# Kernel tuning notes

Measured on AMD Instinct MI355X. Metric: run time of the kernel, lower is better.

## Reference

```python
import jax, jax.numpy as jnp
import numpy as np

B, T, C = 4, 2048, 1024
H, D = 16, 64          # n_head, head_size; H*D == C
FF = 4 * C             # compute_layer_scaling * n_embed
EPS = 1e-5


def layernorm(x, g, b):
    mu = jnp.mean(x, axis=-1, keepdims=True)
    var = jnp.var(x, axis=-1, keepdims=True)
    return (x - mu) * jax.lax.rsqrt(var + EPS) * g + b


def setup_inputs() -> dict:
    key = jax.random.key(0)
    ks = jax.random.split(key, 12)
    s_c = 1.0 / np.sqrt(C)
    s_ff = 1.0 / np.sqrt(FF)
    return {
        "x": jax.random.normal(ks[0], (B, T, C), dtype=jnp.float32),
        # per-head Q/K/V weights, stacked: [H, C, D] (Linear with bias=False)
        "Wq": jax.random.normal(ks[1], (H, C, D), dtype=jnp.float32) * s_c,
        "Wk": jax.random.normal(ks[2], (H, C, D), dtype=jnp.float32) * s_c,
        "Wv": jax.random.normal(ks[3], (H, C, D), dtype=jnp.float32) * s_c,
        "Wproj": jax.random.normal(ks[4], (C, C), dtype=jnp.float32) * s_c,
        "bproj": jnp.zeros((C,), dtype=jnp.float32),
        "W1": jax.random.normal(ks[5], (C, FF), dtype=jnp.float32) * s_c,
        "b1": jnp.zeros((FF,), dtype=jnp.float32),
        "W2": jax.random.normal(ks[6], (FF, FF), dtype=jnp.float32) * s_ff,
        "b2": jnp.zeros((FF,), dtype=jnp.float32),
        "W3": jax.random.normal(ks[7], (FF, C), dtype=jnp.float32) * s_ff,
        "b3": jnp.zeros((C,), dtype=jnp.float32),
        "ln1_g": jnp.ones((C,), dtype=jnp.float32),
        "ln1_b": jnp.zeros((C,), dtype=jnp.float32),
        "ln2_g": jnp.ones((C,), dtype=jnp.float32),
        "ln2_b": jnp.zeros((C,), dtype=jnp.float32),
    }


def reference(x, Wq, Wk, Wv, Wproj, bproj, W1, b1, W2, b2, W3, b3,
              ln1_g, ln1_b, ln2_g, ln2_b):
    # --- multi-head causal self-attention (pre-LN) ---
    h = layernorm(x, ln1_g, ln1_b)
    q = jnp.einsum("btc,hcd->bhtd", h, Wq)
    k = jnp.einsum("btc,hcd->bhtd", h, Wk)
    v = jnp.einsum("btc,hcd->bhtd", h, Wv)
    # NOTE: original scales by n_embed**-0.5 (C from x.shape), not head_size
    scores = jnp.einsum("bhtd,bhsd->bhts", q, k) * (C ** -0.5)
    causal = jnp.tril(jnp.ones((T, T), dtype=bool))
    scores = jnp.where(causal, scores, -jnp.inf)
    wei = jax.nn.softmax(scores, axis=-1)          # dropout p=0 -> identity
    attn = jnp.einsum("bhts,bhsd->bhtd", wei, v)
    attn = attn.transpose(0, 2, 1, 3).reshape(B, T, C)  # concat heads
    x = x + attn @ Wproj + bproj
    # --- feed-forward (pre-LN): C -> FF -> relu -> FF -> relu -> C ---
    h2 = layernorm(x, ln2_g, ln2_b)
    h2 = jax.nn.relu(h2 @ W1 + b1)
    h2 = jax.nn.relu(h2 @ W2 + b2)
    x = x + h2 @ W3 + b3
    return x
```

## Files before the change

### kernel.cpp

```cpp
#include <hip/hip_runtime.h>

typedef __bf16 bf16;
typedef bf16  bf16x8 __attribute__((ext_vector_type(8)));
typedef bf16  bf16x4 __attribute__((ext_vector_type(4)));
typedef float f32x4  __attribute__((ext_vector_type(4)));

#define T_SEQ 2048

__device__ __forceinline__ void gload_lds16(const bf16* g, bf16* l) {
    __builtin_amdgcn_global_load_lds(
        (const __attribute__((address_space(1))) unsigned int*)g,
        (__attribute__((address_space(3))) unsigned int*)l,
        16, 0, 0);
}

#define VMCNT(n) asm volatile("s_waitcnt vmcnt(" #n ")" ::: "memory")
#define BAR() do { asm volatile("" ::: "memory"); __builtin_amdgcn_s_barrier(); \
                   asm volatile("" ::: "memory"); } while (0)

__global__ __launch_bounds__(256) void transpose_f32_bf16(
    const float* __restrict__ in, bf16* __restrict__ out, int R, int Cc, int ldo)
{
    __shared__ float tile[32][33];
    const int bx = blockIdx.x * 32;
    const int by = blockIdx.y * 32;
    const long bi = (long)blockIdx.z * R * Cc;
    const long bo = (long)blockIdx.z * Cc * ldo;
    const int tx = threadIdx.x, ty = threadIdx.y;
#pragma unroll
    for (int i = 0; i < 4; ++i)
        tile[ty + i * 8][tx] = in[bi + (long)(by + ty + i * 8) * Cc + bx + tx];
    __syncthreads();
#pragma unroll
    for (int i = 0; i < 4; ++i)
        out[bo + (long)(bx + ty + i * 8) * ldo + by + tx] = (bf16)tile[tx][ty + i * 8];
}

__global__ __launch_bounds__(256) void transpose_bf16(
    const bf16* __restrict__ in, bf16* __restrict__ out, int ldi, int ldo)
{
    __shared__ bf16 tile[32][33];
    const int bx = blockIdx.x * 32;
    const int by = blockIdx.y * 32;
    const int tx = threadIdx.x, ty = threadIdx.y;
#pragma unroll
    for (int i = 0; i < 4; ++i)
        tile[ty + i * 8][tx] = in[(long)(by + ty + i * 8) * ldi + bx + tx];
    __syncthreads();
#pragma unroll
    for (int i = 0; i < 4; ++i)
        out[(long)(bx + ty + i * 8) * ldo + by + tx] = tile[tx][ty + i * 8];
}

__global__ __launch_bounds__(256) void ln_kernel(
    const float* __restrict__ x, const float* __restrict__ g,
    const float* __restrict__ bb, bf16* __restrict__ out)
{
    const long row = blockIdx.x;
    const int tid = threadIdx.x;
    const float4 v = ((const float4*)(x + row * 1024))[tid];
    float s  = v.x + v.y + v.z + v.w;
    float s2 = v.x * v.x + v.y * v.y + v.z * v.z + v.w * v.w;
#pragma unroll
    for (int off = 32; off >= 1; off >>= 1) {
        s  += __shfl_xor(s,  off, 64);
        s2 += __shfl_xor(s2, off, 64);
    }
    __shared__ float red[8];
    const int wid = tid >> 6;
    if ((tid & 63) == 0) { red[wid] = s; red[4 + wid] = s2; }
    __syncthreads();
    s  = red[0] + red[1] + red[2] + red[3];
    s2 = red[4] + red[5] + red[6] + red[7];
    const float mu   = s * (1.f / 1024.f);
    const float rstd = rsqrtf(s2 * (1.f / 1024.f) - mu * mu + 1e-5f);
    const float4 gv = ((const float4*)g)[tid];
    const float4 bv = ((const float4*)bb)[tid];
    bf16x4 ov;
    ov[0] = (bf16)((v.x - mu) * rstd * gv.x + bv.x);
    ov[1] = (bf16)((v.y - mu) * rstd * gv.y + bv.y);
    ov[2] = (bf16)((v.z - mu) * rstd * gv.z + bv.z);
    ov[3] = (bf16)((v.w - mu) * rstd * gv.w + bv.w);
    *(bf16x4*)(out + row * 1024 + tid * 4) = ov;
}

__global__ __launch_bounds__(256) void ln_kernel_b(
    const bf16* __restrict__ x, const float* __restrict__ g,
    const float* __restrict__ bb, bf16* __restrict__ out)
{
    const long row = blockIdx.x;
    const int tid = threadIdx.x;
    const bf16x4 vb = ((const bf16x4*)(x + row * 1024))[tid];
    const float v0 = (float)vb[0], v1 = (float)vb[1];
    const float v2 = (float)vb[2], v3 = (float)vb[3];
    float s  = v0 + v1 + v2 + v3;
    float s2 = v0 * v0 + v1 * v1 + v2 * v2 + v3 * v3;
#pragma unroll
    for (int off = 32; off >= 1; off >>= 1) {
        s  += __shfl_xor(s,  off, 64);
        s2 += __shfl_xor(s2, off, 64);
    }
    __shared__ float red[8];
    const int wid = tid >> 6;
    if ((tid & 63) == 0) { red[wid] = s; red[4 + wid] = s2; }
    __syncthreads();
    s  = red[0] + red[1] + red[2] + red[3];
    s2 = red[4] + red[5] + red[6] + red[7];
    const float mu   = s * (1.f / 1024.f);
    const float rstd = rsqrtf(s2 * (1.f / 1024.f) - mu * mu + 1e-5f);
    const float4 gv = ((const float4*)g)[tid];
    const float4 bv = ((const float4*)bb)[tid];
    bf16x4 ov;
    ov[0] = (bf16)((v0 - mu) * rstd * gv.x + bv.x);
    ov[1] = (bf16)((v1 - mu) * rstd * gv.y + bv.y);
    ov[2] = (bf16)((v2 - mu) * rstd * gv.z + bv.z);
    ov[3] = (bf16)((v3 - mu) * rstd * gv.w + bv.w);
    *(bf16x4*)(out + row * 1024 + tid * 4) = ov;
}

#define LOADA(BUFP, QM) do {                                                   \
    const char* ab_ = (BUFP) + (size_t)((wr * 64 + (QM) * 128 + fr) * 128);    \
    _Pragma("unroll") for (int m_ = 0; m_ < 4; ++m_) {                         \
        af[m_][0] = *(const bf16x8*)(ab_ + m_ * 2048 + so0);                   \
        af[m_][1] = *(const bf16x8*)(ab_ + m_ * 2048 + so1); } } while (0)

#define LOADB(BUFP, QN, DST) do {                                              \
    const char* bb_ = (BUFP) + (size_t)((wc * 32 + (QN) * 128 + fr) * 128);    \
    _Pragma("unroll") for (int n_ = 0; n_ < 2; ++n_) {                         \
        DST[n_][0] = *(const bf16x8*)(bb_ + n_ * 2048 + so0);                  \
        DST[n_][1] = *(const bf16x8*)(bb_ + n_ * 2048 + so1); } } while (0)

#define MMA(ACC, BSET) do { __builtin_amdgcn_s_setprio(1);                     \
    _Pragma("unroll") for (int m_ = 0; m_ < 4; ++m_)                           \
    _Pragma("unroll") for (int n_ = 0; n_ < 2; ++n_) {                         \
        ACC[m_][n_] = __builtin_amdgcn_mfma_f32_16x16x32_bf16(                 \
            af[m_][0], BSET[n_][0], ACC[m_][n_], 0, 0, 0);                     \
        ACC[m_][n_] = __builtin_amdgcn_mfma_f32_16x16x32_bf16(                 \
            af[m_][1], BSET[n_][1], ACC[m_][n_], 0, 0, 0); }                   \
    __builtin_amdgcn_s_setprio(0); } while (0)

#define TB_DEEP(W1N, W3N, ISSN, ISSC) do {                                     \
    const char* abuf = cAs + ((size_t)cur << 15);                              \
    const char* bbuf = cBs + ((size_t)cur << 15);                              \
    const long kb  = (long)(k + 1) * 64;                                       \
    const long kb2 = (long)(k + 2) * 64;                                       \
    LOADA(abuf, 0);                                                            \
    LOADB(bbuf, 0, bfv0);                                                      \
    if (ISSN) stageB(nxt, 0, kb);                                 \
    BAR(); MMA(a00, bfv0); BAR();                                              \
    LOADB(bbuf, 1, bfv1);                                                      \
    if (ISSN) stageA(nxt, 1, kb);                                 \
    VMCNT(W1N);                                                                \
    BAR(); MMA(a01, bfv1); BAR();                                              \
    LOADA(abuf, 1);                                                            \
    if (ISSC) stageA(cur, 0, kb2);                                \
    BAR(); MMA(a11, bfv1); BAR();                                              \
    if (ISSC) stageB(cur, 1, kb2);                                \
    VMCNT(W3N);                                                                \
    BAR(); MMA(a10, bfv0); BAR(); } while (0)

template <int MODE>
__global__ __launch_bounds__(512, 1) void gemm256(
    const bf16* __restrict__ A, const bf16* __restrict__ Bt,
    const float* __restrict__ bias, const float* __restrict__ resid,
    void* __restrict__ outp, int M, int N, int K, int nbn)
{
    extern __shared__ __align__(16) char smem[];
    char* cAs = smem;
    char* cBs = smem + 65536;

    const int tid = threadIdx.x;
    const int wid = tid >> 6, lane = tid & 63;
    const int wr = wid >> 2, wc = wid & 3;
    const int fr = lane & 15, fq = lane >> 4;

    const int nwg = gridDim.x;
    const int cpx = nwg >> 3;
    const int b0  = blockIdx.x;
    const int bid = (b0 & 7) * cpx + (b0 >> 3);
    const long bm = bid / nbn, bn = bid % nbn;
    const long bmrow = bm * 256, bnrow = bn * 256;

    const int srow0 = wid * 8 + (lane >> 3);
    const int sslot = (lane & 7) ^ (lane >> 3);
    auto stageA = [&](int buf, int h, long kt) {
        const bf16* g = A + (size_t)(bmrow + h * 128 + srow0) * K + kt + sslot * 8;
        char* l = cAs + ((size_t)buf << 15) + h * 16384 + (size_t)wid * 1024;
        gload_lds16(g, (bf16*)l);
        gload_lds16(g + (size_t)64 * K, (bf16*)(l + 8192));
    };
    auto stageB = [&](int buf, int h, long kt) {
        const bf16* g = Bt + (size_t)(bnrow + h * 128 + srow0) * K + kt + sslot * 8;
        char* l = cBs + ((size_t)buf << 15) + h * 16384 + (size_t)wid * 1024;
        gload_lds16(g, (bf16*)l);
        gload_lds16(g + (size_t)64 * K, (bf16*)(l + 8192));
    };

    const int sx  = fr & 7;
    const int so0 = ((fq) ^ sx) * 16;
    const int so1 = ((4 + fq) ^ sx) * 16;

    bf16x8 af[4][2], bfv0[2][2], bfv1[2][2];
    f32x4 a00[4][2], a01[4][2], a11[4][2], a10[4][2];
#pragma unroll
    for (int m = 0; m < 4; ++m)
#pragma unroll
        for (int n = 0; n < 2; ++n) {
            a00[m][n] = {0.f, 0.f, 0.f, 0.f}; a01[m][n] = {0.f, 0.f, 0.f, 0.f};
            a11[m][n] = {0.f, 0.f, 0.f, 0.f}; a10[m][n] = {0.f, 0.f, 0.f, 0.f};
        }

    stageA(0, 0, 0);
    stageB(0, 1, 0);
    stageB(0, 0, 0);
    stageA(0, 1, 0);
    stageA(1, 0, 64);
    stageB(1, 1, 64);
    VMCNT(6);
    BAR();

    const int NT = K >> 6;
    int cur, nxt;
    int k = 0;
    for (; k < NT - 2; ++k) {
        cur = k & 1; nxt = cur ^ 1;
        TB_DEEP(8, 6, true, true);
    }
    cur = k & 1; nxt = cur ^ 1;
    TB_DEEP(8, 2, true, false);
    ++k;
    cur = k & 1; nxt = cur ^ 1;
    TB_DEEP(0, 0, false, false);

    auto writeQ = [&](f32x4 (&acc)[4][2], int QM, int QN) {
#pragma unroll
        for (int m = 0; m < 4; ++m) {
            const long row0 = bmrow + wr * 64 + QM * 128 + m * 16 + fq * 4;
#pragma unroll
            for (int n = 0; n < 2; ++n) {
                const long col = bnrow + wc * 32 + QN * 128 + n * 16 + fr;
                const float bv = (MODE == 0) ? 0.f : bias[col];
#pragma unroll
                for (int j = 0; j < 4; ++j) {
                    const long row = row0 + j;
                    float v = acc[m][n][j] + bv;
                    if (MODE == 1) v = fmaxf(v, 0.f);
                    if (MODE == 2) {
                        v += resid[row * N + col];
                        ((float*)outp)[row * N + col] = v;
                    } else {
                        ((bf16*)outp)[row * N + col] = (bf16)v;
                    }
                }
            }
        }
    };
    writeQ(a00, 0, 0); writeQ(a01, 0, 1); writeQ(a11, 1, 1); writeQ(a10, 1, 0);
}

#define TILE_BODY_N(PRE, LAST) do {                                            \
    const char* abuf = cAs + ((size_t)cur << 15);                              \
    const char* bbuf = cBs + ((size_t)cur << 14);                              \
    const long kn = (long)(k + 1) * 64;                                        \
    LOADA(abuf, 0);                                                            \
    LOADB(bbuf, 0, bfv);                                                       \
    if (PRE) { stageA(nxt, 0, kn); stageB(nxt, kn); stageA(nxt, 1, kn);        \
               VMCNT(6); }                                                     \
    else     { VMCNT(0); }                                                     \
    BAR(); MMA(aq0, bfv); BAR();                                               \
    LOADA(abuf, 1);                                                            \
    if (PRE) { VMCNT(2); }                                                     \
    if (!LAST) { BAR(); }                                                      \
    MMA(aq1, bfv);                                                             \
    if (!LAST) { BAR(); } } while (0)

template <int MODE>
__global__ __launch_bounds__(512, 2) void gemm256n(
    const bf16* __restrict__ A, const bf16* __restrict__ Bt,
    const float* __restrict__ bias, const void* __restrict__ resid,
    void* __restrict__ outp, int M, int N, int K, int nbn)
{
    extern __shared__ __align__(16) char smem[];
    char* cAs = smem;
    char* cBs = smem + 65536;

    const int tid = threadIdx.x;
    const int wid = tid >> 6, lane = tid & 63;
    const int wr = wid >> 2, wc = wid & 3;
    const int fr = lane & 15, fq = lane >> 4;

    const int nwg = gridDim.x;
    const int cpx = nwg >> 3;
    const int b0  = blockIdx.x;
    const int bid = (b0 & 7) * cpx + (b0 >> 3);
    const long bm = bid / nbn, bn = bid % nbn;
    const long bmrow = bm * 256, bnrow = bn * 128;

    const int srow0 = wid * 8 + (lane >> 3);
    const int sslot = (lane & 7) ^ (lane >> 3);
    auto stageA = [&](int buf, int h, long kt) {
        const bf16* g = A + (size_t)(bmrow + h * 128 + srow0) * K + kt + sslot * 8;
        char* l = cAs + ((size_t)buf << 15) + h * 16384 + (size_t)wid * 1024;
        gload_lds16(g, (bf16*)l);
        gload_lds16(g + (size_t)64 * K, (bf16*)(l + 8192));
    };
    auto stageB = [&](int buf, long kt) {
        const bf16* g = Bt + (size_t)(bnrow + srow0) * K + kt + sslot * 8;
        char* l = cBs + ((size_t)buf << 14) + (size_t)wid * 1024;
        gload_lds16(g, (bf16*)l);
        gload_lds16(g + (size_t)64 * K, (bf16*)(l + 8192));
    };

    const int sx  = fr & 7;
    const int so0 = ((fq) ^ sx) * 16;
    const int so1 = ((4 + fq) ^ sx) * 16;

    bf16x8 af[4][2], bfv[2][2];
    f32x4 aq0[4][2], aq1[4][2];
#pragma unroll
    for (int m = 0; m < 4; ++m)
#pragma unroll
        for (int n = 0; n < 2; ++n) {
            aq0[m][n] = {0.f, 0.f, 0.f, 0.f};
            aq1[m][n] = {0.f, 0.f, 0.f, 0.f};
        }

    stageA(0, 0, 0); stageB(0, 0); stageA(0, 1, 0);
    VMCNT(2);
    BAR();

    const int NT = K >> 6;
    int cur = 0, nxt = 1;
    int k = 0;
    for (; k < NT - 1; ++k) {
        cur = k & 1; nxt = cur ^ 1;
        TILE_BODY_N(true, false);
    }
    cur = k & 1; nxt = cur ^ 1;
    TILE_BODY_N(false, true);

    auto writeQ = [&](f32x4 (&acc)[4][2], int QM) {
#pragma unroll
        for (int m = 0; m < 4; ++m) {
            const long row0 = bmrow + wr * 64 + QM * 128 + m * 16 + fq * 4;
#pragma unroll
            for (int n = 0; n < 2; ++n) {
                const long col = bnrow + wc * 32 + n * 16 + fr;
                const float bv = (MODE == 0) ? 0.f : bias[col];
#pragma unroll
                for (int j = 0; j < 4; ++j) {
                    const long row = row0 + j;
                    float v = acc[m][n][j] + bv;
                    if (MODE == 3) {
                        v += ((const float*)resid)[row * N + col];
                        ((bf16*)outp)[row * N + col] = (bf16)v;
                    } else if (MODE == 4) {
                        v += (float)((const bf16*)resid)[row * N + col];
                        ((float*)outp)[row * N + col] = v;
                    } else {
                        ((bf16*)outp)[row * N + col] = (bf16)v;
                    }
                }
            }
        }
    };
    writeQ(aq0, 0); writeQ(aq1, 1);
}

__device__ __forceinline__ void sm_part(
    f32x4* s, float* mj, f32x4* o, f32x4& o_l, bf16* Pp,
    int fr, int fq, int qloc, bool diag)
{
    float v[4][4], mxj[4];
#pragma unroll
    for (int j = 0; j < 4; ++j) {
        const int qg = qloc + fq * 4 + j;
        v[0][j] = s[0][j] * 0.03125f;
        v[1][j] = s[1][j] * 0.03125f;
        v[2][j] = s[2][j] * 0.03125f;
        v[3][j] = s[3][j] * 0.03125f;
        if (diag) {
            if (fr      > qg) v[0][j] = -1e30f;
            if (16 + fr > qg) v[1][j] = -1e30f;
            if (32 + fr > qg) v[2][j] = -1e30f;
            if (48 + fr > qg) v[3][j] = -1e30f;
        }
        float mx = fmaxf(fmaxf(v[0][j], v[1][j]), fmaxf(v[2][j], v[3][j]));
#pragma unroll
        for (int off = 1; off <= 8; off <<= 1) mx = fmaxf(mx, __shfl_xor(mx, off, 16));
        mxj[j] = mx;
    }
    float need = fmaxf(fmaxf(mxj[0] - mj[0], mxj[1] - mj[1]),
                       fmaxf(mxj[2] - mj[2], mxj[3] - mj[3]));
    if (__any(need > 8.f)) {
#pragma unroll
        for (int j = 0; j < 4; ++j) {
            const float mn   = fmaxf(mj[j], mxj[j]);
            const float corr = __expf(mj[j] - mn);
            mj[j] = mn;
#pragma unroll
            for (int nd = 0; nd < 4; ++nd) o[nd][j] *= corr;
            o_l[j] *= corr;
        }
    }
#pragma unroll
    for (int j = 0; j < 4; ++j) {
        bf16* prow = Pp + (fq * 4 + j) * 72;
        prow[fr]      = (bf16)__expf(v[0][j] - mj[j]);
        prow[16 + fr] = (bf16)__expf(v[1][j] - mj[j]);
        prow[32 + fr] = (bf16)__expf(v[2][j] - mj[j]);
        prow[48 + fr] = (bf16)__expf(v[3][j] - mj[j]);
    }
}

__device__ __forceinline__ void attn_step(
    const bf16* __restrict__ Ks, const bf16* __restrict__ Vt,
    bf16* __restrict__ Pp, const bf16x8* qf,
    f32x4* o, f32x4& o_l, float* mj, const bf16x8 onesf,
    int fr, int fq, int qloc, bool diag)
{
    f32x4 s[4];
#pragma unroll
    for (int n = 0; n < 4; ++n) s[n] = {0.f, 0.f, 0.f, 0.f};
    __builtin_amdgcn_s_setprio(1);
#pragma unroll
    for (int n = 0; n < 4; ++n) {
        const int t  = n * 16 + fr;
        const int sw = ((t ^ (t >> 3)) & 7) << 4;
        const bf16x8 kf0 = *(const bf16x8*)((const char*)Ks + t * 128 + ((fq * 16) ^ sw));
        const bf16x8 kf1 = *(const bf16x8*)((const char*)Ks + t * 128 + ((64 + fq * 16) ^ sw));
        s[n] = __builtin_amdgcn_mfma_f32_16x16x32_bf16(qf[0], kf0, s[n], 0, 0, 0);
        s[n] = __builtin_amdgcn_mfma_f32_16x16x32_bf16(qf[1], kf1, s[n], 0, 0, 0);
    }
    __builtin_amdgcn_s_setprio(0);
    sm_part(s, mj, o, o_l, Pp, fr, fq, qloc, diag);
    asm volatile("s_waitcnt lgkmcnt(0)" ::: "memory");
    __builtin_amdgcn_sched_barrier(0);
    const bf16x8 pf0 = *(const bf16x8*)(Pp + fr * 72 + fq * 8);
    const bf16x8 pf1 = *(const bf16x8*)(Pp + fr * 72 + 32 + fq * 8);
    __builtin_amdgcn_s_setprio(1);
#pragma unroll
    for (int nd = 0; nd < 4; ++nd) {
        const int dd = nd * 16 + fr;
        const int sw = ((dd ^ (dd >> 3)) & 7) << 4;
        const bf16x8 vf0 = *(const bf16x8*)((const char*)Vt + dd * 128 + ((fq * 16) ^ sw));
        const bf16x8 vf1 = *(const bf16x8*)((const char*)Vt + dd * 128 + ((64 + fq * 16) ^ sw));
        o[nd] = __builtin_amdgcn_mfma_f32_16x16x32_bf16(pf0, vf0, o[nd], 0, 0, 0);
        o[nd] = __builtin_amdgcn_mfma_f32_16x16x32_bf16(pf1, vf1, o[nd], 0, 0, 0);
    }
    o_l = __builtin_amdgcn_mfma_f32_16x16x32_bf16(pf0, onesf, o_l, 0, 0, 0);
    o_l = __builtin_amdgcn_mfma_f32_16x16x32_bf16(pf1, onesf, o_l, 0, 0, 0);
    __builtin_amdgcn_s_setprio(0);
}

__device__ __forceinline__ void attn_step2(
    const bf16* __restrict__ Ks, const bf16* __restrict__ Vt,
    bf16* __restrict__ PpA, bf16* __restrict__ PpB,
    const bf16x8* qfA, const bf16x8* qfB,
    f32x4* oA, f32x4& olA, float* mA,
    f32x4* oB, f32x4& olB, float* mB,
    const bf16x8 onesf, int fr, int fq, int qloc, bool diagA)
{
    f32x4 sA[4], sB[4];
#pragma unroll
    for (int n = 0; n < 4; ++n) { sA[n] = {0.f, 0.f, 0.f, 0.f}; sB[n] = {0.f, 0.f, 0.f, 0.f}; }
    __builtin_amdgcn_s_setprio(1);
#pragma unroll
    for (int n = 0; n < 4; ++n) {
        const int t  = n * 16 + fr;
        const int sw = ((t ^ (t >> 3)) & 7) << 4;
        const bf16x8 kf0 = *(const bf16x8*)((const char*)Ks + t * 128 + ((fq * 16) ^ sw));
        const bf16x8 kf1 = *(const bf16x8*)((const char*)Ks + t * 128 + ((64 + fq * 16) ^ sw));
        sA[n] = __builtin_amdgcn_mfma_f32_16x16x32_bf16(qfA[0], kf0, sA[n], 0, 0, 0);
        sA[n] = __builtin_amdgcn_mfma_f32_16x16x32_bf16(qfA[1], kf1, sA[n], 0, 0, 0);
        sB[n] = __builtin_amdgcn_mfma_f32_16x16x32_bf16(qfB[0], kf0, sB[n], 0, 0, 0);
        sB[n] = __builtin_amdgcn_mfma_f32_16x16x32_bf16(qfB[1], kf1, sB[n], 0, 0, 0);
    }
    __builtin_amdgcn_s_setprio(0);
    sm_part(sA, mA, oA, olA, PpA, fr, fq, qloc, diagA);
    sm_part(sB, mB, oB, olB, PpB, fr, fq, qloc, false);
    asm volatile("s_waitcnt lgkmcnt(0)" ::: "memory");
    __builtin_amdgcn_sched_barrier(0);
    const bf16x8 pfA0 = *(const bf16x8*)(PpA + fr * 72 + fq * 8);
    const bf16x8 pfA1 = *(const bf16x8*)(PpA + fr * 72 + 32 + fq * 8);
    const bf16x8 pfB0 = *(const bf16x8*)(PpB + fr * 72 + fq * 8);
    const bf16x8 pfB1 = *(const bf16x8*)(PpB + fr * 72 + 32 + fq * 8);
    __builtin_amdgcn_s_setprio(1);
#pragma unroll
    for (int nd = 0; nd < 4; ++nd) {
        const int dd = nd * 16 + fr;
        const int sw = ((dd ^ (dd >> 3)) & 7) << 4;
        const bf16x8 vf0 = *(const bf16x8*)((const char*)Vt + dd * 128 + ((fq * 16) ^ sw));
        const bf16x8 vf1 = *(const bf16x8*)((const char*)Vt + dd * 128 + ((64 + fq * 16) ^ sw));
        oA[nd] = __builtin_amdgcn_mfma_f32_16x16x32_bf16(pfA0, vf0, oA[nd], 0, 0, 0);
        oA[nd] = __builtin_amdgcn_mfma_f32_16x16x32_bf16(pfA1, vf1, oA[nd], 0, 0, 0);
        oB[nd] = __builtin_amdgcn_mfma_f32_16x16x32_bf16(pfB0, vf0, oB[nd], 0, 0, 0);
        oB[nd] = __builtin_amdgcn_mfma_f32_16x16x32_bf16(pfB1, vf1, oB[nd], 0, 0, 0);
    }
    olA = __builtin_amdgcn_mfma_f32_16x16x32_bf16(pfA0, onesf, olA, 0, 0, 0);
    olA = __builtin_amdgcn_mfma_f32_16x16x32_bf16(pfA1, onesf, olA, 0, 0, 0);
    olB = __builtin_amdgcn_mfma_f32_16x16x32_bf16(pfB0, onesf, olB, 0, 0, 0);
    olB = __builtin_amdgcn_mfma_f32_16x16x32_bf16(pfB1, onesf, olB, 0, 0, 0);
    __builtin_amdgcn_s_setprio(0);
}

__global__ __launch_bounds__(256) void attn_kernel(
    const bf16* __restrict__ qkv, const bf16* __restrict__ vt,
    bf16* __restrict__ out)
{
    const int pair = blockIdx.x;
    const int h = blockIdx.y, b = blockIdx.z;
    const int tid = threadIdx.x, wid = tid >> 6, lane = tid & 63;
    const int fr = lane & 15, fq = lane >> 4;
    const int jA = pair, jB = 31 - pair;
    const bf16* baseQ = qkv + ((long)b * T_SEQ) * 3072 + h * 64;
    const bf16* baseK = baseQ + 1024;
    const bf16* baseV = vt + (long)(h * 64) * 8192 + (long)b * T_SEQ;

    __shared__ __align__(16) bf16 Ks[2][64 * 64];
    __shared__ __align__(16) bf16 Vs[2][64 * 64];
    __shared__ __align__(16) bf16 Plds[2][4][16 * 72];

    const int qrA = jA * 64 + wid * 16 + fr;
    const int qrB = jB * 64 + wid * 16 + fr;
    bf16x8 qfA[2], qfB[2];
#pragma unroll
    for (int kk = 0; kk < 2; ++kk) {
        qfA[kk] = *(const bf16x8*)(baseQ + (long)qrA * 3072 + kk * 32 + fq * 8);
        qfB[kk] = *(const bf16x8*)(baseQ + (long)qrB * 3072 + kk * 32 + fq * 8);
    }

    bf16x8 onesf;
    {
        const bf16 ov = (fr == 0) ? (bf16)1.f : (bf16)0.f;
#pragma unroll
        for (int e = 0; e < 8; ++e) onesf[e] = ov;
    }

    f32x4 oA[4], oB[4], olA, olB;
    float mA[4], mB[4];
#pragma unroll
    for (int nd = 0; nd < 4; ++nd) { oA[nd] = {0.f, 0.f, 0.f, 0.f}; oB[nd] = {0.f, 0.f, 0.f, 0.f}; }
    olA = {0.f, 0.f, 0.f, 0.f}; olB = {0.f, 0.f, 0.f, 0.f};
#pragma unroll
    for (int j = 0; j < 4; ++j) { mA[j] = -1e30f; mB[j] = -1e30f; }

    const int t_p0 = wid * 16 + (lane >> 3);
    const int t_p1 = t_p0 + 8;
    const int kcb0 = ((lane & 7) * 16) ^ (((t_p0 ^ (t_p0 >> 3)) & 7) << 4);
    const int kcb1 = ((lane & 7) * 16) ^ (((t_p1 ^ (t_p1 >> 3)) & 7) << 4);

    bf16* PA = &Plds[0][wid][0];
    bf16* PB = &Plds[1][wid][0];

    auto stage = [&](int buf, int c) {
        const long s0 = (long)c * 64;
        gload_lds16(baseK + (s0 + t_p0) * 3072 + (kcb0 >> 1), &Ks[buf][(wid * 2) * 512]);
        gload_lds16(baseK + (s0 + t_p1) * 3072 + (kcb1 >> 1), &Ks[buf][(wid * 2 + 1) * 512]);
        gload_lds16(baseV + (long)t_p0 * 8192 + s0 + (kcb0 >> 1), &Vs[buf][(wid * 2) * 512]);
        gload_lds16(baseV + (long)t_p1 * 8192 + s0 + (kcb1 >> 1), &Vs[buf][(wid * 2 + 1) * 512]);
    };

    const int nch = jB + 1;
    stage(0, 0);
    for (int c = 0; c < nch; ++c) {
        const int cur = c & 1;
        if (c + 1 < nch) { stage(cur ^ 1, c + 1); VMCNT(4); }
        else             { VMCNT(0); }
        BAR();
        if (c <= jA)
            attn_step2(Ks[cur], Vs[cur], PA, PB, qfA, qfB,
                       oA, olA, mA, oB, olB, mB, onesf, fr, fq, wid * 16, c == jA);
        else
            attn_step(Ks[cur], Vs[cur], PB, qfB, oB, olB, mB, onesf,
                      fr, fq, wid * 16, c == jB);
        BAR();
    }

#pragma unroll
    for (int j = 0; j < 4; ++j) {
        const float lA = __shfl(olA[j], lane & 48, 64);
        const float lB = __shfl(olB[j], lane & 48, 64);
        const float rA = 1.f / lA, rB = 1.f / lB;
        const long rowA = (long)b * T_SEQ + jA * 64 + wid * 16 + fq * 4 + j;
        const long rowB = (long)b * T_SEQ + jB * 64 + wid * 16 + fq * 4 + j;
#pragma unroll
        for (int nd = 0; nd < 4; ++nd) {
            out[rowA * 1024 + h * 64 + nd * 16 + fr] = (bf16)(oA[nd][j] * rA);
            out[rowB * 1024 + h * 64 + nd * 16 + fr] = (bf16)(oB[nd][j] * rB);
        }
    }
}

extern "C" void kernel_launch(void* const* d_in, const int* in_sizes, int n_in,
                              void* d_out, int out_size, void* d_ws, size_t ws_size,
                              hipStream_t stream)
{
    const float* x     = (const float*)d_in[0];
    const float* Wq    = (const float*)d_in[1];
    const float* Wk    = (const float*)d_in[2];
    const float* Wv    = (const float*)d_in[3];
    const float* Wproj = (const float*)d_in[4];
    const float* bproj = (const float*)d_in[5];
    const float* W1    = (const float*)d_in[6];
    const float* b1    = (const float*)d_in[7];
    const float* W2    = (const float*)d_in[8];
    const float* b2    = (const float*)d_in[9];
    const float* W3    = (const float*)d_in[10];
    const float* b3    = (const float*)d_in[11];
    const float* ln1g  = (const float*)d_in[12];
    const float* ln1b  = (const float*)d_in[13];
    const float* ln2g  = (const float*)d_in[14];
    const float* ln2b  = (const float*)d_in[15];

    char* ws = (char*)d_ws;
    size_t off = 0;
    auto alloc = [&](size_t bytes) {
        void* p = ws + off;
        off += (bytes + 255) & ~(size_t)255;
        return p;
    };
    bf16* Wqkv_t  = (bf16*)alloc(3072ul * 1024 * 2);
    bf16* Wproj_t = (bf16*)alloc(1024ul * 1024 * 2);
    bf16* W1_t    = (bf16*)alloc(4096ul * 1024 * 2);
    bf16* W2_t    = (bf16*)alloc(4096ul * 4096 * 2);
    bf16* W3_t    = (bf16*)alloc(1024ul * 4096 * 2);
    bf16* hbuf    = (bf16*)alloc(8192ul * 1024 * 2);
    bf16* x1b     = (bf16*)alloc(8192ul * 1024 * 2);
    bf16* a1      = (bf16*)alloc(8192ul * 4096 * 2);
    char* R1      = (char*)alloc(8192ul * 4096 * 2);
    bf16* qkvb    = (bf16*)R1;
    bf16* attnb   = (bf16*)(R1 + 8192ul * 3072 * 2);
    bf16* a2      = (bf16*)R1;
    bf16* vt      = a1;

    hipFuncSetAttribute(reinterpret_cast<const void*>(&gemm256<1>),
                        hipFuncAttributeMaxDynamicSharedMemorySize, 131072);
    hipFuncSetAttribute(reinterpret_cast<const void*>(&gemm256n<0>),
                        hipFuncAttributeMaxDynamicSharedMemorySize, 98304);
    hipFuncSetAttribute(reinterpret_cast<const void*>(&gemm256n<3>),
                        hipFuncAttributeMaxDynamicSharedMemorySize, 98304);
    hipFuncSetAttribute(reinterpret_cast<const void*>(&gemm256n<4>),
                        hipFuncAttributeMaxDynamicSharedMemorySize, 98304);

    const dim3 tb(32, 8);
    transpose_f32_bf16<<<dim3(2, 32, 16), tb, 0, stream>>>(Wq, Wqkv_t,                1024, 64, 1024);
    transpose_f32_bf16<<<dim3(2, 32, 16), tb, 0, stream>>>(Wk, Wqkv_t + 1024l * 1024, 1024, 64, 1024);
    transpose_f32_bf16<<<dim3(2, 32, 16), tb, 0, stream>>>(Wv, Wqkv_t + 2048l * 1024, 1024, 64, 1024);
    transpose_f32_bf16<<<dim3(32, 32, 1),   tb, 0, stream>>>(Wproj, Wproj_t, 1024, 1024, 1024);
    transpose_f32_bf16<<<dim3(128, 32, 1),  tb, 0, stream>>>(W1, W1_t, 1024, 4096, 1024);
    transpose_f32_bf16<<<dim3(128, 128, 1), tb, 0, stream>>>(W2, W2_t, 4096, 4096, 4096);
    transpose_f32_bf16<<<dim3(32, 128, 1),  tb, 0, stream>>>(W3, W3_t, 4096, 1024, 4096);

    ln_kernel<<<8192, 256, 0, stream>>>(x, ln1g, ln1b, hbuf);
    gemm256n<0><<<768, 512, 98304, stream>>>(hbuf, Wqkv_t, nullptr, nullptr, qkvb,
                                             8192, 3072, 1024, 24);
    transpose_bf16<<<dim3(32, 256), tb, 0, stream>>>(qkvb + 2048, vt, 3072, 8192);
    attn_kernel<<<dim3(16, 16, 4), 256, 0, stream>>>(qkvb, vt, attnb);
    gemm256n<3><<<256, 512, 98304, stream>>>(attnb, Wproj_t, bproj, x, x1b,
                                             8192, 1024, 1024, 8);
    ln_kernel_b<<<8192, 256, 0, stream>>>(x1b, ln2g, ln2b, hbuf);
    gemm256<1><<<512, 512, 131072, stream>>>(hbuf, W1_t, b1, nullptr, a1,
                                             8192, 4096, 1024, 16);
    gemm256<1><<<512, 512, 131072, stream>>>(a1, W2_t, b2, nullptr, a2,
                                             8192, 4096, 4096, 16);
    gemm256n<4><<<256, 512, 98304, stream>>>(a2, W3_t, b3, x1b, (float*)d_out,
                                             8192, 1024, 4096, 8);
}
```

Baseline: 665.5 us.

## Split paired causal attention blocks into one query tile per block, swizzle P

The attention kernel previously gave each block two query tiles (jA, 31-jA) so every block had equal causal work, and shared each K/V chunk between the two. It now launches one block per query tile, ordered longest first, which doubles the grid and lets more blocks run concurrently, at the cost of loading each K/V chunk once per tile instead of once per pair. The P staging buffer in LDS changes from a padded 72-element stride to a 128-byte XOR-swizzled layout, aiming to cut bank conflicts and LDS footprint.

```diff
diff --git a/kernel.cpp b/kernel.cpp
--- a/kernel.cpp
+++ b/kernel.cpp
@@ -367,10 +367,26 @@
     writeQ(aq0, 0); writeQ(aq1, 1);
 }
 
-__device__ __forceinline__ void sm_part(
-    f32x4* s, float* mj, f32x4* o, f32x4& o_l, bf16* Pp,
+__device__ __forceinline__ void attn_step(
+    const bf16* __restrict__ Ks, const bf16* __restrict__ Vt,
+    bf16* __restrict__ Pp, const bf16x8* qf,
+    f32x4* o, f32x4& o_l, float* mj, const bf16x8 onesf,
     int fr, int fq, int qloc, bool diag)
 {
+    f32x4 s[4];
+#pragma unroll
+    for (int n = 0; n < 4; ++n) s[n] = {0.f, 0.f, 0.f, 0.f};
+    __builtin_amdgcn_s_setprio(1);
+#pragma unroll
+    for (int n = 0; n < 4; ++n) {
+        const int t  = n * 16 + fr;
+        const int sw = ((t ^ (t >> 3)) & 7) << 4;
+        const bf16x8 kf0 = *(const bf16x8*)((const char*)Ks + t * 128 + ((fq * 16) ^ sw));
+        const bf16x8 kf1 = *(const bf16x8*)((const char*)Ks + t * 128 + ((64 + fq * 16) ^ sw));
+        s[n] = __builtin_amdgcn_mfma_f32_16x16x32_bf16(qf[0], kf0, s[n], 0, 0, 0);
+        s[n] = __builtin_amdgcn_mfma_f32_16x16x32_bf16(qf[1], kf1, s[n], 0, 0, 0);
+    }
+    __builtin_amdgcn_s_setprio(0);
     float v[4][4], mxj[4];
 #pragma unroll
     for (int j = 0; j < 4; ++j) {
@@ -405,39 +421,19 @@
     }
 #pragma unroll
     for (int j = 0; j < 4; ++j) {
-        bf16* prow = Pp + (fq * 4 + j) * 72;
-        prow[fr]      = (bf16)__expf(v[0][j] - mj[j]);
-        prow[16 + fr] = (bf16)__expf(v[1][j] - mj[j]);
-        prow[32 + fr] = (bf16)__expf(v[2][j] - mj[j]);
-        prow[48 + fr] = (bf16)__expf(v[3][j] - mj[j]);
-    }
-}
-
-__device__ __forceinline__ void attn_step(
-    const bf16* __restrict__ Ks, const bf16* __restrict__ Vt,
-    bf16* __restrict__ Pp, const bf16x8* qf,
-    f32x4* o, f32x4& o_l, float* mj, const bf16x8 onesf,
-    int fr, int fq, int qloc, bool diag)
-{
-    f32x4 s[4];
-#pragma unroll
-    for (int n = 0; n < 4; ++n) s[n] = {0.f, 0.f, 0.f, 0.f};
-    __builtin_amdgcn_s_setprio(1);
-#pragma unroll
-    for (int n = 0; n < 4; ++n) {
-        const int t  = n * 16 + fr;
-        const int sw = ((t ^ (t >> 3)) & 7) << 4;
-        const bf16x8 kf0 = *(const bf16x8*)((const char*)Ks + t * 128 + ((fq * 16) ^ sw));
-        const bf16x8 kf1 = *(const bf16x8*)((const char*)Ks + t * 128 + ((64 + fq * 16) ^ sw));
-        s[n] = __builtin_amdgcn_mfma_f32_16x16x32_bf16(qf[0], kf0, s[n], 0, 0, 0);
-        s[n] = __builtin_amdgcn_mfma_f32_16x16x32_bf16(qf[1], kf1, s[n], 0, 0, 0);
-    }
-    __builtin_amdgcn_s_setprio(0);
-    sm_part(s, mj, o, o_l, Pp, fr, fq, qloc, diag);
+        const int r = fq * 4 + j;
+        char* prow = (char*)Pp + r * 128;
+        const int sw = (r & 7) << 4;
+        *(bf16*)(prow + ((fr * 2) ^ sw))      = (bf16)__expf(v[0][j] - mj[j]);
+        *(bf16*)(prow + ((32 + fr * 2) ^ sw)) = (bf16)__expf(v[1][j] - mj[j]);
+        *(bf16*)(prow + ((64 + fr * 2) ^ sw)) = (bf16)__expf(v[2][j] - mj[j]);
+        *(bf16*)(prow + ((96 + fr * 2) ^ sw)) = (bf16)__expf(v[3][j] - mj[j]);
+    }
     asm volatile("s_waitcnt lgkmcnt(0)" ::: "memory");
     __builtin_amdgcn_sched_barrier(0);
-    const bf16x8 pf0 = *(const bf16x8*)(Pp + fr * 72 + fq * 8);
-    const bf16x8 pf1 = *(const bf16x8*)(Pp + fr * 72 + 32 + fq * 8);
+    const int swr = (fr & 7) << 4;
+    const bf16x8 pf0 = *(const bf16x8*)((const char*)Pp + fr * 128 + ((fq * 16) ^ swr));
+    const bf16x8 pf1 = *(const bf16x8*)((const char*)Pp + fr * 128 + ((64 + fq * 16) ^ swr));
     __builtin_amdgcn_s_setprio(1);
 #pragma unroll
     for (int nd = 0; nd < 4; ++nd) {
@@ -453,82 +449,27 @@
     __builtin_amdgcn_s_setprio(0);
 }
 
-__device__ __forceinline__ void attn_step2(
-    const bf16* __restrict__ Ks, const bf16* __restrict__ Vt,
-    bf16* __restrict__ PpA, bf16* __restrict__ PpB,
-    const bf16x8* qfA, const bf16x8* qfB,
-    f32x4* oA, f32x4& olA, float* mA,
-    f32x4* oB, f32x4& olB, float* mB,
-    const bf16x8 onesf, int fr, int fq, int qloc, bool diagA)
-{
-    f32x4 sA[4], sB[4];
-#pragma unroll
-    for (int n = 0; n < 4; ++n) { sA[n] = {0.f, 0.f, 0.f, 0.f}; sB[n] = {0.f, 0.f, 0.f, 0.f}; }
-    __builtin_amdgcn_s_setprio(1);
-#pragma unroll
-    for (int n = 0; n < 4; ++n) {
-        const int t  = n * 16 + fr;
-        const int sw = ((t ^ (t >> 3)) & 7) << 4;
-        const bf16x8 kf0 = *(const bf16x8*)((const char*)Ks + t * 128 + ((fq * 16) ^ sw));
-        const bf16x8 kf1 = *(const bf16x8*)((const char*)Ks + t * 128 + ((64 + fq * 16) ^ sw));
-        sA[n] = __builtin_amdgcn_mfma_f32_16x16x32_bf16(qfA[0], kf0, sA[n], 0, 0, 0);
-        sA[n] = __builtin_amdgcn_mfma_f32_16x16x32_bf16(qfA[1], kf1, sA[n], 0, 0, 0);
-        sB[n] = __builtin_amdgcn_mfma_f32_16x16x32_bf16(qfB[0], kf0, sB[n], 0, 0, 0);
-        sB[n] = __builtin_amdgcn_mfma_f32_16x16x32_bf16(qfB[1], kf1, sB[n], 0, 0, 0);
-    }
-    __builtin_amdgcn_s_setprio(0);
-    sm_part(sA, mA, oA, olA, PpA, fr, fq, qloc, diagA);
-    sm_part(sB, mB, oB, olB, PpB, fr, fq, qloc, false);
-    asm volatile("s_waitcnt lgkmcnt(0)" ::: "memory");
-    __builtin_amdgcn_sched_barrier(0);
-    const bf16x8 pfA0 = *(const bf16x8*)(PpA + fr * 72 + fq * 8);
-    const bf16x8 pfA1 = *(const bf16x8*)(PpA + fr * 72 + 32 + fq * 8);
-    const bf16x8 pfB0 = *(const bf16x8*)(PpB + fr * 72 + fq * 8);
-    const bf16x8 pfB1 = *(const bf16x8*)(PpB + fr * 72 + 32 + fq * 8);
-    __builtin_amdgcn_s_setprio(1);
-#pragma unroll
-    for (int nd = 0; nd < 4; ++nd) {
-        const int dd = nd * 16 + fr;
-        const int sw = ((dd ^ (dd >> 3)) & 7) << 4;
-        const bf16x8 vf0 = *(const bf16x8*)((const char*)Vt + dd * 128 + ((fq * 16) ^ sw));
-        const bf16x8 vf1 = *(const bf16x8*)((const char*)Vt + dd * 128 + ((64 + fq * 16) ^ sw));
-        oA[nd] = __builtin_amdgcn_mfma_f32_16x16x32_bf16(pfA0, vf0, oA[nd], 0, 0, 0);
-        oA[nd] = __builtin_amdgcn_mfma_f32_16x16x32_bf16(pfA1, vf1, oA[nd], 0, 0, 0);
-        oB[nd] = __builtin_amdgcn_mfma_f32_16x16x32_bf16(pfB0, vf0, oB[nd], 0, 0, 0);
-        oB[nd] = __builtin_amdgcn_mfma_f32_16x16x32_bf16(pfB1, vf1, oB[nd], 0, 0, 0);
-    }
-    olA = __builtin_amdgcn_mfma_f32_16x16x32_bf16(pfA0, onesf, olA, 0, 0, 0);
-    olA = __builtin_amdgcn_mfma_f32_16x16x32_bf16(pfA1, onesf, olA, 0, 0, 0);
-    olB = __builtin_amdgcn_mfma_f32_16x16x32_bf16(pfB0, onesf, olB, 0, 0, 0);
-    olB = __builtin_amdgcn_mfma_f32_16x16x32_bf16(pfB1, onesf, olB, 0, 0, 0);
-    __builtin_amdgcn_s_setprio(0);
-}
-
 __global__ __launch_bounds__(256) void attn_kernel(
     const bf16* __restrict__ qkv, const bf16* __restrict__ vt,
     bf16* __restrict__ out)
 {
-    const int pair = blockIdx.x;
+    const int jq = 31 - blockIdx.x;
     const int h = blockIdx.y, b = blockIdx.z;
     const int tid = threadIdx.x, wid = tid >> 6, lane = tid & 63;
     const int fr = lane & 15, fq = lane >> 4;
-    const int jA = pair, jB = 31 - pair;
     const bf16* baseQ = qkv + ((long)b * T_SEQ) * 3072 + h * 64;
     const bf16* baseK = baseQ + 1024;
     const bf16* baseV = vt + (long)(h * 64) * 8192 + (long)b * T_SEQ;
 
     __shared__ __align__(16) bf16 Ks[2][64 * 64];
     __shared__ __align__(16) bf16 Vs[2][64 * 64];
-    __shared__ __align__(16) bf16 Plds[2][4][16 * 72];
-
-    const int qrA = jA * 64 + wid * 16 + fr;
-    const int qrB = jB * 64 + wid * 16 + fr;
-    bf16x8 qfA[2], qfB[2];
-#pragma unroll
-    for (int kk = 0; kk < 2; ++kk) {
-        qfA[kk] = *(const bf16x8*)(baseQ + (long)qrA * 3072 + kk * 32 + fq * 8);
-        qfB[kk] = *(const bf16x8*)(baseQ + (long)qrB * 3072 + kk * 32 + fq * 8);
-    }
+    __shared__ __align__(16) bf16 Pl[4][1024];
+
+    const int qr = jq * 64 + wid * 16 + fr;
+    bf16x8 qf[2];
+#pragma unroll
+    for (int kk = 0; kk < 2; ++kk)
+        qf[kk] = *(const bf16x8*)(baseQ + (long)qr * 3072 + kk * 32 + fq * 8);
 
     bf16x8 onesf;
     {
@@ -537,21 +478,20 @@
         for (int e = 0; e < 8; ++e) onesf[e] = ov;
     }
 
-    f32x4 oA[4], oB[4], olA, olB;
-    float mA[4], mB[4];
-#pragma unroll
-    for (int nd = 0; nd < 4; ++nd) { oA[nd] = {0.f, 0.f, 0.f, 0.f}; oB[nd] = {0.f, 0.f, 0.f, 0.f}; }
-    olA = {0.f, 0.f, 0.f, 0.f}; olB = {0.f, 0.f, 0.f, 0.f};
-#pragma unroll
-    for (int j = 0; j < 4; ++j) { mA[j] = -1e30f; mB[j] = -1e30f; }
+    f32x4 o[4], ol;
+    float mj[4];
+#pragma unroll
+    for (int nd = 0; nd < 4; ++nd) o[nd] = {0.f, 0.f, 0.f, 0.f};
+    ol = {0.f, 0.f, 0.f, 0.f};
+#pragma unroll
+    for (int j = 0; j < 4; ++j) mj[j] = -1e30f;
 
     const int t_p0 = wid * 16 + (lane >> 3);
     const int t_p1 = t_p0 + 8;
     const int kcb0 = ((lane & 7) * 16) ^ (((t_p0 ^ (t_p0 >> 3)) & 7) << 4);
     const int kcb1 = ((lane & 7) * 16) ^ (((t_p1 ^ (t_p1 >> 3)) & 7) << 4);
 
-    bf16* PA = &Plds[0][wid][0];
-    bf16* PB = &Plds[1][wid][0];
+    bf16* P = &Pl[wid][0];
 
     auto stage = [&](int buf, int c) {
         const long s0 = (long)c * 64;
@@ -561,34 +501,26 @@
         gload_lds16(baseV + (long)t_p1 * 8192 + s0 + (kcb1 >> 1), &Vs[buf][(wid * 2 + 1) * 512]);
     };
 
-    const int nch = jB + 1;
+    const int nch = jq + 1;
     stage(0, 0);
     for (int c = 0; c < nch; ++c) {
         const int cur = c & 1;
         if (c + 1 < nch) { stage(cur ^ 1, c + 1); VMCNT(4); }
         else             { VMCNT(0); }
         BAR();
-        if (c <= jA)
-            attn_step2(Ks[cur], Vs[cur], PA, PB, qfA, qfB,
-                       oA, olA, mA, oB, olB, mB, onesf, fr, fq, wid * 16, c == jA);
-        else
-            attn_step(Ks[cur], Vs[cur], PB, qfB, oB, olB, mB, onesf,
-                      fr, fq, wid * 16, c == jB);
+        attn_step(Ks[cur], Vs[cur], P, qf, o, ol, mj, onesf,
+                  fr, fq, wid * 16, c == jq);
         BAR();
     }
 
 #pragma unroll
     for (int j = 0; j < 4; ++j) {
-        const float lA = __shfl(olA[j], lane & 48, 64);
-        const float lB = __shfl(olB[j], lane & 48, 64);
-        const float rA = 1.f / lA, rB = 1.f / lB;
-        const long rowA = (long)b * T_SEQ + jA * 64 + wid * 16 + fq * 4 + j;
-        const long rowB = (long)b * T_SEQ + jB * 64 + wid * 16 + fq * 4 + j;
-#pragma unroll
-        for (int nd = 0; nd < 4; ++nd) {
-            out[rowA * 1024 + h * 64 + nd * 16 + fr] = (bf16)(oA[nd][j] * rA);
-            out[rowB * 1024 + h * 64 + nd * 16 + fr] = (bf16)(oB[nd][j] * rB);
-        }
+        const float l = __shfl(ol[j], lane & 48, 64);
+        const float r = 1.f / l;
+        const long row = (long)b * T_SEQ + jq * 64 + wid * 16 + fq * 4 + j;
+#pragma unroll
+        for (int nd = 0; nd < 4; ++nd)
+            out[row * 1024 + h * 64 + nd * 16 + fr] = (bf16)(o[nd][j] * r);
     }
 }
 
@@ -656,7 +588,7 @@
     gemm256n<0><<<768, 512, 98304, stream>>>(hbuf, Wqkv_t, nullptr, nullptr, qkvb,
                                              8192, 3072, 1024, 24);
     transpose_bf16<<<dim3(32, 256), tb, 0, stream>>>(qkvb + 2048, vt, 3072, 8192);
-    attn_kernel<<<dim3(16, 16, 4), 256, 0, stream>>>(qkvb, vt, attnb);
+    attn_kernel<<<dim3(32, 16, 4), 256, 0, stream>>>(qkvb, vt, attnb);
     gemm256n<3><<<256, 512, 98304, stream>>>(attnb, Wproj_t, bproj, x, x1b,
                                              8192, 1024, 1024, 8);
     ln_kernel_b<<<8192, 256, 0, stream>>>(x1b, ln2g, ln2b, hbuf);
```

Result: slower. 705.3 us (+6.0%).
